# Performance work log

Measured on AMD Instinct MI355X. Metric: run time of the kernel, lower is better.

Reference implementation:

```python
import jax, jax.numpy as jnp
import numpy as np

B, T, D = 2, 2048, 2048
H, KV = 16, 4
HD = D // H            # 128
REP = H // KV          # 4 query heads per kv head


def setup_inputs() -> dict:
    key = jax.random.key(0)
    ks = jax.random.split(key, 5)
    scale = D ** -0.5
    x = jax.random.normal(ks[0], (B, T, D), dtype=jnp.float32)
    Wq = jax.random.normal(ks[1], (D, H * HD), dtype=jnp.float32) * scale
    Wk = jax.random.normal(ks[2], (D, KV * HD), dtype=jnp.float32) * scale
    Wv = jax.random.normal(ks[3], (D, KV * HD), dtype=jnp.float32) * scale
    Wo = jax.random.normal(ks[4], (H * HD, D), dtype=jnp.float32) * scale
    return {"x": x, "Wq": Wq, "Wk": Wk, "Wv": Wv, "Wo": Wo}


def reference(x, Wq, Wk, Wv, Wo):
    b, t, d = x.shape
    # projections; group query heads by their kv head (repeat_interleave order:
    # q head h uses kv head h // REP, i.e. heads are contiguous per group)
    q = (x @ Wq).reshape(b, t, KV, REP, HD)          # bt(g r)d -> b t g r d
    k = (x @ Wk).reshape(b, t, KV, HD)
    v = (x @ Wv).reshape(b, t, KV, HD)
    # scores: [B, KV, REP, T, T] -- equivalent to repeat_interleave of kv heads
    scores = jnp.einsum('btgrd,bsgd->bgrts', q, k) * (HD ** -0.5)
    causal = jnp.tril(jnp.ones((t, t), dtype=bool))
    scores = jnp.where(causal, scores, -jnp.inf)
    weights = jax.nn.softmax(scores, axis=-1)
    out = jnp.einsum('bgrts,bsgd->btgrd', weights, v).reshape(b, t, H * HD)
    return jnp.round(out @ Wo, decimals=4)
```

## Files before the change

### kernel.cpp

```cpp
#include <hip/hip_runtime.h>
#include <hip/hip_bf16.h>
#include <math.h>

#define B_ 2
#define T_ 2048
#define D_ 2048
#define H_ 16
#define KV_ 4
#define HD_ 128
#define REP_ 4
#define QKVSTR 3072

typedef __attribute__((ext_vector_type(8))) short s16x8;
typedef __attribute__((ext_vector_type(4))) short s16x4;
typedef __attribute__((ext_vector_type(4))) float f32x4;
typedef __attribute__((ext_vector_type(16))) float f32x16;
typedef __hip_bfloat16 bf16;

__device__ __forceinline__ short f2bf(float x) {
    bf16 h = __float2bfloat16(x);
    return *reinterpret_cast<short*>(&h);
}

__device__ __forceinline__ void gl2lds16(const void* g, void* l) {
    __builtin_amdgcn_global_load_lds(
        (const __attribute__((address_space(1))) char*)g,
        (__attribute__((address_space(3))) char*)l, 16, 0, 0);
}

__global__ __launch_bounds__(256) void prep(const float* __restrict__ x,
                                            const float* __restrict__ Wq,
                                            const float* __restrict__ Wk,
                                            const float* __restrict__ Wv,
                                            const float* __restrict__ Wo,
                                            bf16* __restrict__ xb,
                                            bf16* __restrict__ Wqkvt,
                                            bf16* __restrict__ Wot,
                                            float qscale) {
    const int bid = blockIdx.x;
    const int t = threadIdx.x;
    if (bid < 4096) {
        int i = (bid * 256 + t) * 8;
        float4 a = *(const float4*)(x + i);
        float4 b = *(const float4*)(x + i + 4);
        short o[8] = {f2bf(a.x), f2bf(a.y), f2bf(a.z), f2bf(a.w),
                      f2bf(b.x), f2bf(b.y), f2bf(b.z), f2bf(b.w)};
        *(s16x8*)(xb + i) = *(const s16x8*)o;
        return;
    }
    __shared__ short tile[64 * 72];
    const float* W; bf16* dst; int N; float scale; int seg;
    if (bid < 5120)      { seg = bid - 4096; W = Wq; dst = Wqkvt;                      N = 2048; scale = qscale; }
    else if (bid < 5376) { seg = bid - 5120; W = Wk; dst = Wqkvt + (size_t)2048 * D_;  N = 512;  scale = 1.f; }
    else if (bid < 5632) { seg = bid - 5376; W = Wv; dst = Wqkvt + (size_t)2560 * D_;  N = 512;  scale = 1.f; }
    else                 { seg = bid - 5632; W = Wo; dst = Wot;                        N = 2048; scale = 1.f; }
    const int k0 = (seg & 31) * 64, n0 = (seg >> 5) * 64;
    const int r = t >> 2, c0 = (t & 3) * 16;
    const float* src = W + (size_t)(k0 + r) * N + n0 + c0;
    #pragma unroll
    for (int i = 0; i < 16; i += 4) {
        float4 v = *(const float4*)(src + i);
        tile[r * 72 + c0 + i + 0] = f2bf(v.x * scale);
        tile[r * 72 + c0 + i + 1] = f2bf(v.y * scale);
        tile[r * 72 + c0 + i + 2] = f2bf(v.z * scale);
        tile[r * 72 + c0 + i + 3] = f2bf(v.w * scale);
    }
    __syncthreads();
    short tmp[16];
    #pragma unroll
    for (int i = 0; i < 16; ++i) tmp[i] = tile[(c0 + i) * 72 + r];
    bf16* d = dst + (size_t)(n0 + r) * D_ + k0 + c0;
    *(s16x8*)(d)     = *(const s16x8*)&tmp[0];
    *(s16x8*)(d + 8) = *(const s16x8*)&tmp[8];
}

template<typename OUTT, int ROUND, int WVT>
__global__ __launch_bounds__(256, 3) void gemm_nt(const bf16* __restrict__ A,
                                                  const bf16* __restrict__ Bt,
                                                  OUTT* __restrict__ C,
                                                  bf16* __restrict__ Vtg,
                                                  int M, int N, int K) {
    __shared__ short As[128 * 64];
    __shared__ short Bs[128 * 64];
    const int tid = threadIdx.x;
    const int lane = tid & 63;
    const int wave = tid >> 6;
    const int quad = lane >> 4;
    const int l16 = lane & 15;
    const int wr = wave >> 1, wc = wave & 1;
    const int row0 = blockIdx.y * 128;
    const int col0 = blockIdx.x * 128;

    f32x4 acc[4][4] = {};

    for (int k0 = 0; k0 < K; k0 += 64) {
        __syncthreads();
        #pragma unroll
        for (int i = 0; i < 4; ++i) {
            int g = i * 256 + tid;
            int row = g >> 3;
            int cs = (g & 7) ^ (row & 7);
            gl2lds16(A + (size_t)(row0 + row) * K + k0 + cs * 8, &As[g * 8]);
        }
        #pragma unroll
        for (int i = 0; i < 4; ++i) {
            int g = i * 256 + tid;
            int row = g >> 3;
            int cs = (g & 7) ^ (row & 7);
            gl2lds16(Bt + (size_t)(col0 + row) * K + k0 + cs * 8, &Bs[g * 8]);
        }
        __syncthreads();
        #pragma unroll
        for (int kk = 0; kk < 2; ++kk) {
            s16x8 af[4], bfr[4];
            #pragma unroll
            for (int i = 0; i < 4; ++i) {
                int row = wr * 64 + i * 16 + l16;
                int c = (kk * 4 + quad) ^ (row & 7);
                af[i] = *(const s16x8*)&As[row * 64 + c * 8];
            }
            #pragma unroll
            for (int j = 0; j < 4; ++j) {
                int row = wc * 64 + j * 16 + l16;
                int c = (kk * 4 + quad) ^ (row & 7);
                bfr[j] = *(const s16x8*)&Bs[row * 64 + c * 8];
            }
            #pragma unroll
            for (int i = 0; i < 4; ++i)
                #pragma unroll
                for (int j = 0; j < 4; ++j)
                    acc[i][j] = __builtin_amdgcn_mfma_f32_16x16x32_bf16(
                        af[i], bfr[j], acc[i][j], 0, 0, 0);
        }
    }

    #pragma unroll
    for (int i = 0; i < 4; ++i) {
        #pragma unroll
        for (int j = 0; j < 4; ++j) {
            const int col = col0 + wc * 64 + j * 16 + l16;
            const int rowb = row0 + wr * 64 + i * 16 + quad * 4;
            #pragma unroll
            for (int r = 0; r < 4; ++r) {
                float v = acc[i][j][r];
                if (ROUND) v = rintf(v * 1e4f) * 1e-4f;
                if constexpr (sizeof(OUTT) == 2)
                    C[(size_t)(rowb + r) * N + col] = __float2bfloat16(v);
                else
                    C[(size_t)(rowb + r) * N + col] = v;
            }
            if constexpr (WVT) {
                if (col >= 2560) {
                    const int dcol = (col - 2560) & 127;
                    const int g = (col - 2560) >> 7;
                    const int b = rowb >> 11;
                    const int t = rowb & 2047;
                    short pk[4] = {f2bf(acc[i][j][0]), f2bf(acc[i][j][1]),
                                   f2bf(acc[i][j][2]), f2bf(acc[i][j][3])};
                    *(s16x4*)&Vtg[(size_t)((b * KV_ + g) * HD_ + dcol) * T_ + t] =
                        *(const s16x4*)pk;
                }
            }
        }
    }
}

__global__ __launch_bounds__(256, 2) void flash9(const bf16* __restrict__ Q,
                                                 const bf16* __restrict__ K,
                                                 const bf16* __restrict__ Vtg,
                                                 bf16* __restrict__ O) {
    __shared__ short smem[32768];

    const int h = blockIdx.x;
    const int b = blockIdx.y & 1;
    const int qt = 15 - (blockIdx.y >> 1);
    const int g = h >> 2;
    const int tid = threadIdx.x;
    const int lane = tid & 63;
    const int wave = tid >> 6;
    const int l32 = lane & 31;
    const int hi = lane >> 5;
    const int qw0 = qt * 128 + wave * 32;
    const int qg = qw0 + l32;

    s16x8 qf[8];
    {
        const bf16* qp = Q + (size_t)(b * T_ + qg) * QKVSTR + h * HD_ + hi * 8;
        #pragma unroll
        for (int kt = 0; kt < 8; ++kt) qf[kt] = *(const s16x8*)(qp + kt * 16);
    }

    const bf16* Kp = K + (size_t)(b * T_) * QKVSTR + g * HD_;
    const bf16* Vp = Vtg + (size_t)((b * KV_ + g) * HD_) * T_;

    float l_part = 0.f;
    f32x16 oacc[4] = {};

    const int jmax = 2 * qt + 1;

    #pragma unroll
    for (int i = 0; i < 4; ++i) {
        int g2 = i * 256 + tid;
        int s = g2 >> 4;
        int cs = (g2 & 15) ^ (s & 15);
        gl2lds16(Kp + (size_t)s * QKVSTR + cs * 8, &smem[g2 * 8]);
    }
    #pragma unroll
    for (int i = 0; i < 4; ++i) {
        int g2 = i * 256 + tid;
        int d = g2 >> 3;
        int cs = (g2 & 7) ^ (d & 7);
        gl2lds16(Vp + (size_t)d * T_ + cs * 8, &smem[8192 + g2 * 8]);
    }

    for (int j = 0; j <= jmax; ++j) {
        const int kb = (j & 1) << 14;
        __syncthreads();

        if (j < jmax) {
            const int s0n = (j + 1) * 64;
            const int nb = ((j + 1) & 1) << 14;
            #pragma unroll
            for (int i = 0; i < 4; ++i) {
                int g2 = i * 256 + tid;
                int s = g2 >> 4;
                int cs = (g2 & 15) ^ (s & 15);
                gl2lds16(Kp + (size_t)(s0n + s) * QKVSTR + cs * 8, &smem[nb + g2 * 8]);
            }
            #pragma unroll
            for (int i = 0; i < 4; ++i) {
                int g2 = i * 256 + tid;
                int d = g2 >> 3;
                int cs = (g2 & 7) ^ (d & 7);
                gl2lds16(Vp + (size_t)d * T_ + s0n + cs * 8, &smem[nb + 8192 + g2 * 8]);
            }
        }

        const int s0 = j * 64;
        if (s0 >= qw0 + 32) continue;

        f32x16 sacc[2] = {};
        #pragma unroll
        for (int kt = 0; kt < 8; ++kt) {
            #pragma unroll
            for (int mt = 0; mt < 2; ++mt) {
                int s = mt * 32 + l32;
                int c = (kt * 2 + hi) ^ (s & 15);
                const s16x8 kf = *(const s16x8*)&smem[kb + s * 128 + c * 8];
                sacc[mt] = __builtin_amdgcn_mfma_f32_32x32x16_bf16(
                    kf, qf[kt], sacc[mt], 0, 0, 0);
            }
        }

        const bool diagw = (s0 + 63 > qw0);
        #pragma unroll
        for (int mt = 0; mt < 2; ++mt) {
            #pragma unroll
            for (int r = 0; r < 16; ++r) {
                float sv = sacc[mt][r];
                if (diagw) {
                    int sg = s0 + mt * 32 + (r & 3) + 8 * (r >> 2) + 4 * hi;
                    if (sg > qg) sv = -INFINITY;
                }
                float e = exp2f(sv);
                sacc[mt][r] = e;
                l_part += e;
            }
            #pragma unroll
            for (int kts = 0; kts < 2; ++kts) {
                const int o = kts * 8;
                unsigned w01, w23, w45, w67;
                asm("v_cvt_pk_bf16_f32 %0, %1, %2"
                    : "=v"(w01) : "v"(sacc[mt][o + 0]), "v"(sacc[mt][o + 1]));
                asm("v_cvt_pk_bf16_f32 %0, %1, %2"
                    : "=v"(w23) : "v"(sacc[mt][o + 2]), "v"(sacc[mt][o + 3]));
                asm("v_cvt_pk_bf16_f32 %0, %1, %2"
                    : "=v"(w45) : "v"(sacc[mt][o + 4]), "v"(sacc[mt][o + 5]));
                asm("v_cvt_pk_bf16_f32 %0, %1, %2"
                    : "=v"(w67) : "v"(sacc[mt][o + 6]), "v"(sacc[mt][o + 7]));
                asm("v_permlane32_swap_b32 %0, %1" : "+v"(w01), "+v"(w45));
                asm("v_permlane32_swap_b32 %0, %1" : "+v"(w23), "+v"(w67));
                union { unsigned u[4]; s16x8 v; } pu;
                pu.u[0] = w01; pu.u[1] = w23; pu.u[2] = w45; pu.u[3] = w67;
                const s16x8 pa = pu.v;
                #pragma unroll
                for (int nt = 0; nt < 4; ++nt) {
                    int d = nt * 32 + l32;
                    int c = ((mt * 2 + kts) * 2 + hi) ^ (d & 7);
                    const s16x8 vf = *(const s16x8*)&smem[kb + 8192 + d * 64 + c * 8];
                    oacc[nt] = __builtin_amdgcn_mfma_f32_32x32x16_bf16(
                        pa, vf, oacc[nt], 0, 0, 0);
                }
            }
        }
    }

    l_part += __shfl_xor(l_part, 32);
    const float invl = 1.f / l_part;

    bf16* op = O + (size_t)(b * T_ + qw0) * (H_ * HD_) + h * HD_;
    #pragma unroll
    for (int r = 0; r < 16; ++r) {
        const int qrow = (r & 3) + 8 * (r >> 2) + 4 * hi;
        const float il = __shfl(invl, qrow);
        #pragma unroll
        for (int nt = 0; nt < 4; ++nt)
            op[(size_t)qrow * (H_ * HD_) + nt * 32 + l32] =
                __float2bfloat16(oacc[nt][r] * il);
    }
}

extern "C" void kernel_launch(void* const* d_in, const int* in_sizes, int n_in,
                              void* d_out, int out_size, void* d_ws, size_t ws_size,
                              hipStream_t stream) {
    const float* x  = (const float*)d_in[0];
    const float* Wq = (const float*)d_in[1];
    const float* Wk = (const float*)d_in[2];
    const float* Wv = (const float*)d_in[3];
    const float* Wo = (const float*)d_in[4];
    float* out = (float*)d_out;

    const size_t NR = (size_t)B_ * T_;
    bf16* ws = (bf16*)d_ws;
    bf16* xb    = ws;
    bf16* Wqkvt = xb + NR * D_;
    bf16* Wot   = Wqkvt + (size_t)QKVSTR * D_;
    bf16* QKVb  = Wot + (size_t)D_ * D_;
    bf16* Vtg   = QKVb + NR * QKVSTR;
    bf16* Ab    = Vtg + (size_t)B_ * KV_ * HD_ * T_;

    const float qscale = 1.4426950408889634f / sqrtf((float)HD_);

    prep<<<6656, 256, 0, stream>>>(x, Wq, Wk, Wv, Wo, xb, Wqkvt, Wot, qscale);

    gemm_nt<bf16, 0, 1><<<dim3(QKVSTR / 128, NR / 128), 256, 0, stream>>>(
        xb, Wqkvt, QKVb, Vtg, (int)NR, QKVSTR, D_);

    flash9<<<dim3(H_, 32), 256, 0, stream>>>(QKVb, QKVb + 2048, Vtg, Ab);

    gemm_nt<float, 1, 0><<<dim3(D_ / 128, NR / 128), 256, 0, stream>>>(
        Ab, Wot, out, nullptr, (int)NR, D_, H_ * HD_);
}
```

Baseline: 276.4 us.

## Replace GEMM with 8-wave double-buffered LDS pipeline and larger tiles

The old 4-wave 128x128 GEMM used one LDS buffer with a sync before and after each load. The new kernel uses 512 threads, larger tiles (256x256 for the QKV projection, 128x256 for the output projection) and two LDS buffers. The next k-tile is loaded while the current one is computed, using manual vmcnt waits, and MFMA blocks get raised wave priority. This is meant to hide global-load latency and reuse each loaded tile more. In exchange, LDS use per block and register pressure go up, and the grid has fewer blocks.

```diff
diff --git a/kernel.cpp b/kernel.cpp
--- a/kernel.cpp
+++ b/kernel.cpp
@@ -74,72 +74,97 @@
     *(s16x8*)(d + 8) = *(const s16x8*)&tmp[8];
 }
 
-template<typename OUTT, int ROUND, int WVT>
-__global__ __launch_bounds__(256, 3) void gemm_nt(const bf16* __restrict__ A,
-                                                  const bf16* __restrict__ Bt,
-                                                  OUTT* __restrict__ C,
-                                                  bf16* __restrict__ Vtg,
-                                                  int M, int N, int K) {
-    __shared__ short As[128 * 64];
-    __shared__ short Bs[128 * 64];
+template<int MI, int LA, typename OUTT, int ROUND, int WVT>
+__global__ __launch_bounds__(512, 2) void gemm8(const bf16* __restrict__ A,
+                                                const bf16* __restrict__ Bt,
+                                                OUTT* __restrict__ C,
+                                                bf16* __restrict__ Vtg,
+                                                int M, int N, int K) {
+    constexpr int ASZ = MI * 2048;
+    constexpr int BSZ = 16384;
+    __shared__ short smem[2 * (ASZ + BSZ)];
     const int tid = threadIdx.x;
     const int lane = tid & 63;
     const int wave = tid >> 6;
     const int quad = lane >> 4;
     const int l16 = lane & 15;
-    const int wr = wave >> 1, wc = wave & 1;
-    const int row0 = blockIdx.y * 128;
-    const int col0 = blockIdx.x * 128;
-
-    f32x4 acc[4][4] = {};
-
-    for (int k0 = 0; k0 < K; k0 += 64) {
-        __syncthreads();
-        #pragma unroll
-        for (int i = 0; i < 4; ++i) {
-            int g = i * 256 + tid;
+    const int wr = wave >> 2, wc = wave & 3;
+    const int row0 = blockIdx.y * (MI * 32);
+    const int col0 = blockIdx.x * 256;
+    const int NT = K >> 6;
+
+    f32x4 acc[MI][4] = {};
+
+    const bf16* Ap = A + (size_t)row0 * K;
+    const bf16* Bp = Bt + (size_t)col0 * K;
+
+    auto stage = [&](int t) {
+        const int bo = (t & 1) * (ASZ + BSZ);
+        const int k0 = t * 64;
+        #pragma unroll
+        for (int i = 0; i < LA; ++i) {
+            int g = i * 512 + tid;
             int row = g >> 3;
             int cs = (g & 7) ^ (row & 7);
-            gl2lds16(A + (size_t)(row0 + row) * K + k0 + cs * 8, &As[g * 8]);
+            gl2lds16(Ap + (size_t)row * K + k0 + cs * 8, &smem[bo + g * 8]);
         }
         #pragma unroll
         for (int i = 0; i < 4; ++i) {
-            int g = i * 256 + tid;
+            int g = i * 512 + tid;
             int row = g >> 3;
             int cs = (g & 7) ^ (row & 7);
-            gl2lds16(Bt + (size_t)(col0 + row) * K + k0 + cs * 8, &Bs[g * 8]);
-        }
-        __syncthreads();
+            gl2lds16(Bp + (size_t)row * K + k0 + cs * 8, &smem[bo + ASZ + g * 8]);
+        }
+    };
+
+    stage(0);
+    for (int t = 0; t < NT; ++t) {
+        if (t + 1 < NT) {
+            stage(t + 1);
+            if constexpr (LA == 4) asm volatile("s_waitcnt vmcnt(8)" ::: "memory");
+            else                   asm volatile("s_waitcnt vmcnt(6)" ::: "memory");
+        } else {
+            asm volatile("s_waitcnt vmcnt(0)" ::: "memory");
+        }
+        __builtin_amdgcn_s_barrier();
+        asm volatile("" ::: "memory");
+
+        const int bo = (t & 1) * (ASZ + BSZ);
         #pragma unroll
         for (int kk = 0; kk < 2; ++kk) {
-            s16x8 af[4], bfr[4];
-            #pragma unroll
-            for (int i = 0; i < 4; ++i) {
-                int row = wr * 64 + i * 16 + l16;
+            s16x8 af[MI], bfr[4];
+            #pragma unroll
+            for (int i = 0; i < MI; ++i) {
+                int row = wr * (MI * 16) + i * 16 + l16;
                 int c = (kk * 4 + quad) ^ (row & 7);
-                af[i] = *(const s16x8*)&As[row * 64 + c * 8];
+                af[i] = *(const s16x8*)&smem[bo + row * 64 + c * 8];
             }
             #pragma unroll
             for (int j = 0; j < 4; ++j) {
                 int row = wc * 64 + j * 16 + l16;
                 int c = (kk * 4 + quad) ^ (row & 7);
-                bfr[j] = *(const s16x8*)&Bs[row * 64 + c * 8];
-            }
-            #pragma unroll
-            for (int i = 0; i < 4; ++i)
+                bfr[j] = *(const s16x8*)&smem[bo + ASZ + row * 64 + c * 8];
+            }
+            __builtin_amdgcn_s_setprio(1);
+            #pragma unroll
+            for (int i = 0; i < MI; ++i)
                 #pragma unroll
                 for (int j = 0; j < 4; ++j)
                     acc[i][j] = __builtin_amdgcn_mfma_f32_16x16x32_bf16(
                         af[i], bfr[j], acc[i][j], 0, 0, 0);
-        }
-    }
-
-    #pragma unroll
-    for (int i = 0; i < 4; ++i) {
+            __builtin_amdgcn_s_setprio(0);
+        }
+        asm volatile("s_waitcnt lgkmcnt(0)" ::: "memory");
+        __builtin_amdgcn_s_barrier();
+        asm volatile("" ::: "memory");
+    }
+
+    #pragma unroll
+    for (int i = 0; i < MI; ++i) {
         #pragma unroll
         for (int j = 0; j < 4; ++j) {
             const int col = col0 + wc * 64 + j * 16 + l16;
-            const int rowb = row0 + wr * 64 + i * 16 + quad * 4;
+            const int rowb = row0 + wr * (MI * 16) + i * 16 + quad * 4;
             #pragma unroll
             for (int r = 0; r < 4; ++r) {
                 float v = acc[i][j][r];
@@ -333,11 +358,11 @@
 
     prep<<<6656, 256, 0, stream>>>(x, Wq, Wk, Wv, Wo, xb, Wqkvt, Wot, qscale);
 
-    gemm_nt<bf16, 0, 1><<<dim3(QKVSTR / 128, NR / 128), 256, 0, stream>>>(
+    gemm8<8, 4, bf16, 0, 1><<<dim3(QKVSTR / 256, NR / 256), 512, 0, stream>>>(
         xb, Wqkvt, QKVb, Vtg, (int)NR, QKVSTR, D_);
 
     flash9<<<dim3(H_, 32), 256, 0, stream>>>(QKVb, QKVb + 2048, Vtg, Ab);
 
-    gemm_nt<float, 1, 0><<<dim3(D_ / 128, NR / 128), 256, 0, stream>>>(
+    gemm8<4, 2, float, 1, 0><<<dim3(D_ / 256, NR / 128), 512, 0, stream>>>(
         Ab, Wot, out, nullptr, (int)NR, D_, H_ * HD_);
 }
```

After: 287.4 us. 4.0% more time.
